# Performance work log

Hardware: AMD Instinct MI355X
Metric: run time of the kernel (lower is better)

The kernel has to match this reference:

```python
import jax, jax.numpy as jnp
import numpy as np

INPUT_SIZE = 512
HIDDEN = 1024
N_QP = 64
M_QP = 128
QP_ITER = 50
MIN_EIG = 0.01
N_P = N_QP * (N_QP + 1) // 2              # 2080
N_H = M_QP * N_QP                          # 8192
N_OUT = N_P + N_QP + N_H + M_QP            # 10464
BATCH = 1024


def setup_inputs() -> dict:
    key = jax.random.key(0)
    ks = jax.random.split(key, 4)
    s = lambda fan_in: np.float32(1.0 / np.sqrt(fan_in))
    return {
        "x": jax.random.normal(ks[0], (BATCH, INPUT_SIZE), jnp.float32),
        "W1": jax.random.normal(ks[1], (INPUT_SIZE, HIDDEN), jnp.float32) * s(INPUT_SIZE),
        "b1": jnp.zeros((HIDDEN,), jnp.float32),
        "W2": jax.random.normal(ks[2], (HIDDEN, HIDDEN), jnp.float32) * s(HIDDEN),
        "b2": jnp.zeros((HIDDEN,), jnp.float32),
        "W3": jax.random.normal(ks[3], (HIDDEN, N_OUT), jnp.float32) * s(HIDDEN),
        "b3": jnp.zeros((N_OUT,), jnp.float32),
    }


def _make_psd(p):
    # p: (bs, n(n+1)/2) packed row-major lower triangle of Cholesky factor L.
    # Diagonal entries (index i(i+1)/2 - 1) -> sqrt(min_eig) + softplus, so P = L L' is PSD.
    bs = p.shape[0]
    i = jnp.arange(1, N_QP + 1)
    diag_idx = i * (i + 1) // 2 - 1
    p = p.at[:, diag_idx].set(np.float32(np.sqrt(MIN_EIG)) + jax.nn.softplus(p[:, diag_idx]))
    r, c = jnp.tril_indices(N_QP)
    L = jnp.zeros((bs, N_QP, N_QP), p.dtype).at[:, r, c].set(p)
    return jnp.einsum('bik,bjk->bij', L, L)


def _forward(x, W1, b1, W2, b2, W3, b3):
    # MLP generating QP parameters (P, q, H, b)
    h = jax.nn.relu(x @ W1 + b1)
    h = jax.nn.relu(h @ W2 + b2)
    out = h @ W3 + b3                               # (bs, N_OUT)
    P_params = out[:, :N_P]
    q = out[:, N_P:N_P + N_QP]                      # (bs, n)
    H = out[:, N_P + N_QP:N_P + N_QP + N_H].reshape(-1, M_QP, N_QP)  # (bs, m, n)
    b = out[:, N_P + N_QP + N_H:]                   # (bs, m)
    P = _make_psd(P_params)                         # (bs, n, n)

    # Step sizes: tau = sigma = 0.9 / ||H||_2, spectral norm via 10 fixed power iterations
    v = jnp.ones((x.shape[0], N_QP), x.dtype) / np.float32(np.sqrt(N_QP))
    for _ in range(10):
        w = jnp.einsum('bmn,bm->bn', H, jnp.einsum('bmn,bn->bm', H, v))
        v = w / (jnp.linalg.norm(w, axis=1, keepdims=True) + 1e-12)
    sn = jnp.linalg.norm(jnp.einsum('bmn,bn->bm', H, v), axis=1) + 1e-6
    tau = (0.9 / sn)[:, None]                       # (bs, 1) primal step
    sig = tau                                       # dual step

    # Precompute (I + tau P)^{-1} once; fixed across PDHG iterations
    eye = jnp.eye(N_QP, dtype=x.dtype)
    Minv = jnp.linalg.inv(eye[None] + tau[:, :, None] * P)

    x0 = jnp.zeros((x.shape[0], N_QP), x.dtype)
    lam0 = jnp.zeros((x.shape[0], M_QP), x.dtype)

    def step(carry, _):
        xp, xbar, lam = carry
        lam = jax.nn.relu(lam - sig * (jnp.einsum('bmn,bn->bm', H, xbar) + b))
        xn = jnp.einsum('bnk,bk->bn', Minv, xp + tau * (jnp.einsum('bmn,bm->bn', H, lam) - q))
        return (xn, 2.0 * xn - xp, lam), None

    (xs, _, _), _ = jax.lax.scan(step, (x0, x0, lam0), None, length=QP_ITER)
    return xs  # (bs, n_qp): last primal iterate, matching solver(...)[1][:, -1, :]


def reference(x, W1, b1, W2, b2, W3, b3):
    return _forward(x, W1, b1, W2, b2, W3, b3)
```

## Files before the change

### kernel.cpp

```cpp
#include <hip/hip_runtime.h>
#include <cstdint>

typedef unsigned short u16;
typedef __attribute__((ext_vector_type(8))) short short8;
typedef __attribute__((ext_vector_type(4))) float floatx4;
typedef __attribute__((ext_vector_type(4))) float f4;

#define NQP   64
#define MQP   128
#define NP    2080
#define NHH   8192
#define NOUT  10464
#define NOUTP 10496

__device__ __forceinline__ float b2f(u16 u) {
  union { unsigned int i; float f; } v; v.i = ((unsigned int)u) << 16; return v.f;
}
__device__ __forceinline__ u16 f2b(float f) {
  union { float f; unsigned int i; } v; v.f = f;
  unsigned int r = v.i + 0x7fffu + ((v.i >> 16) & 1u);
  return (u16)(r >> 16);
}

__global__ __launch_bounds__(256) void detect_dtype(const u16* __restrict__ w,
                                                    int* __restrict__ flag) {
  __shared__ int cnt;
  if (threadIdx.x == 0) cnt = 0;
  __syncthreads();
  int c = 0;
  for (int i = threadIdx.x; i < 16384; i += 256) {
    const int e = (w[i] >> 7) & 0xFF;
    if (e >= 130 || e <= 90) ++c;
  }
  atomicAdd(&cnt, c);
  __syncthreads();
  if (threadIdx.x == 0) flag[0] = (cnt > 3000) ? 1 : 0;
}

__device__ __forceinline__ u16 load_elem_bf16(const void* p, size_t idx, int isf32) {
  return isf32 ? f2b(((const float*)p)[idx]) : ((const u16*)p)[idx];
}

__global__ __launch_bounds__(256) void convert_bf16(const void* __restrict__ in,
                                                    u16* __restrict__ out, int n,
                                                    const int* __restrict__ flag) {
  const int isf = flag[0];
  for (int i = blockIdx.x * 256 + threadIdx.x; i < n; i += gridDim.x * 256)
    out[i] = load_elem_bf16(in, i, isf);
}

__global__ __launch_bounds__(256) void conv_biases(const void* __restrict__ b1,
                                                   const void* __restrict__ b2,
                                                   const void* __restrict__ b3,
                                                   float* __restrict__ bf1,
                                                   float* __restrict__ bf2,
                                                   float* __restrict__ bf3,
                                                   const int* __restrict__ flag) {
  const int isf = flag[0];
  const int i = blockIdx.x * 256 + threadIdx.x;
  if (i < 1024) {
    bf1[i] = isf ? ((const float*)b1)[i] : b2f(((const u16*)b1)[i]);
  } else if (i < 2048) {
    const int j = i - 1024;
    bf2[j] = isf ? ((const float*)b2)[j] : b2f(((const u16*)b2)[j]);
  } else if (i < 2048 + NOUT) {
    const int j = i - 2048;
    bf3[j] = isf ? ((const float*)b3)[j] : b2f(((const u16*)b3)[j]);
  }
}

__global__ __launch_bounds__(256) void transpose_all(const void* __restrict__ W1,
                                                     const void* __restrict__ W2,
                                                     const void* __restrict__ W3,
                                                     u16* __restrict__ W1t,
                                                     u16* __restrict__ W2t,
                                                     u16* __restrict__ W3t,
                                                     const int* __restrict__ flag) {
  const int bx = blockIdx.x, by = blockIdx.y;
  const void* in; u16* out; int K, N, Npad, bxo;
  if (bx < 32)      { in = W1; out = W1t; K = 512;  N = 1024; Npad = 1024;  bxo = 0;
                      if (by >= 16) return; }
  else if (bx < 64) { in = W2; out = W2t; K = 1024; N = 1024; Npad = 1024;  bxo = 32; }
  else              { in = W3; out = W3t; K = 1024; N = NOUT; Npad = NOUTP; bxo = 64; }
  __shared__ u16 tile[32][33];
  const int isf = flag[0];
  const int n0 = (bx - bxo) * 32, k0 = by * 32;
  const int tx = threadIdx.x & 31, ty = threadIdx.x >> 5;
#pragma unroll
  for (int i = 0; i < 4; ++i) {
    const int k = k0 + ty + 8 * i, n = n0 + tx;
    tile[ty + 8 * i][tx] = (n < N) ? load_elem_bf16(in, (size_t)k * N + n, isf) : (u16)0;
  }
  __syncthreads();
#pragma unroll
  for (int i = 0; i < 4; ++i) {
    const int n = n0 + ty + 8 * i, k = k0 + tx;
    if (n < Npad) out[(size_t)n * K + k] = tile[tx][ty + 8 * i];
  }
}

__device__ __forceinline__ void gload_lds16(const u16* g, u16* l) {
  __builtin_amdgcn_global_load_lds((const __attribute__((address_space(1))) void*)g,
                                   (__attribute__((address_space(3))) void*)l, 16, 0, 0);
}

template <int EPI, bool HAS_LO>
__global__ __launch_bounds__(256) void gemm_bt(const u16* __restrict__ Ahi, const u16* __restrict__ Alo,
                                               const u16* __restrict__ Bt,  const float* __restrict__ bias,
                                               u16* __restrict__ Chi, u16* __restrict__ Clo,
                                               float* __restrict__ Cf,
                                               int M, int N, int K) {
  __shared__ __align__(16) u16 lA[128 * 32];
  __shared__ __align__(16) u16 lAlo[128 * 32];
  __shared__ __align__(16) u16 lB[128 * 32];
  const int tile_n = blockIdx.x * 128;
  const int tile_m = blockIdx.y * 128;
  const int lane = threadIdx.x & 63;
  const int wv   = threadIdx.x >> 6;
  const int wm = (wv & 1) * 64;
  const int wn = (wv >> 1) * 64;
  const int sr = lane >> 2;
  const int sk = (lane & 3) * 8;
  floatx4 acc[4][4] = {};

  for (int k0 = 0; k0 < K; k0 += 32) {
#pragma unroll
    for (int it = 0; it < 2; ++it) {
      const int slot = it * 4 + wv;
      const int r = slot * 16 + sr;
      gload_lds16(Ahi + (size_t)(tile_m + r) * K + k0 + sk, lA + slot * 512);
      if (HAS_LO)
        gload_lds16(Alo + (size_t)(tile_m + r) * K + k0 + sk, lAlo + slot * 512);
      gload_lds16(Bt + (size_t)(tile_n + r) * K + k0 + sk, lB + slot * 512);
    }
    __syncthreads();
    const int ro = lane & 15;
    const int qo = (lane >> 4) * 8;
    short8 af[4], bfr[4], al[4];
#pragma unroll
    for (int i = 0; i < 4; ++i) af[i] = *(const short8*)(lA + (wm + i * 16 + ro) * 32 + qo);
#pragma unroll
    for (int j = 0; j < 4; ++j) bfr[j] = *(const short8*)(lB + (wn + j * 16 + ro) * 32 + qo);
    if (HAS_LO) {
#pragma unroll
      for (int i = 0; i < 4; ++i) al[i] = *(const short8*)(lAlo + (wm + i * 16 + ro) * 32 + qo);
    }
#pragma unroll
    for (int i = 0; i < 4; ++i)
#pragma unroll
      for (int j = 0; j < 4; ++j) {
        acc[i][j] = __builtin_amdgcn_mfma_f32_16x16x32_bf16(af[i], bfr[j], acc[i][j], 0, 0, 0);
        if (HAS_LO)
          acc[i][j] = __builtin_amdgcn_mfma_f32_16x16x32_bf16(al[i], bfr[j], acc[i][j], 0, 0, 0);
      }
    __syncthreads();
  }

  const int colb = tile_n + wn + (lane & 15);
  const int rowb = tile_m + wm + (lane >> 4) * 4;
#pragma unroll
  for (int j = 0; j < 4; ++j) {
    const int col = colb + j * 16;
    const float bv = (col < N) ? bias[col] : 0.f;
#pragma unroll
    for (int i = 0; i < 4; ++i) {
#pragma unroll
      for (int v = 0; v < 4; ++v) {
        const int row = rowb + i * 16 + v;
        float val = acc[i][j][v] + bv;
        if (EPI == 0) {
          val = fmaxf(val, 0.f);
          const u16 hi = f2b(val);
          const float lo = val - b2f(hi);
          Chi[(size_t)row * N + col] = hi;
          Clo[(size_t)row * N + col] = f2b(lo);
        } else {
          if (col < N) Cf[(size_t)row * N + col] = val;
        }
      }
    }
  }
}

__device__ __forceinline__ f4 ld4s(const float* p) { return *(const f4*)p; }
__device__ __forceinline__ void st4s(float* p, f4 v) { *(f4*)p = v; }
__device__ __forceinline__ float dot4(f4 a, f4 b) {
  return fmaf(a.x, b.x, fmaf(a.y, b.y, fmaf(a.z, b.z, a.w * b.w)));
}
__device__ __forceinline__ f4 shx4(f4 v, int m) {
  f4 r;
  r.x = __shfl_xor(v.x, m, 64); r.y = __shfl_xor(v.y, m, 64);
  r.z = __shfl_xor(v.z, m, 64); r.w = __shfl_xor(v.w, m, 64);
  return r;
}
__device__ __forceinline__ int hQ(int m, int g) {
  return (m << 6) + (((g ^ (m & 15))) << 2);
}

__global__ __launch_bounds__(256, 4) void qp_solve(const float* __restrict__ outbuf,
                                                   void* __restrict__ xs,
                                                   const int* __restrict__ flag) {
  __shared__ __align__(16) float H_s[8192];
  __shared__ __align__(16) float lam_s[128];
  __shared__ __align__(16) float b_s[128];
  __shared__ __align__(16) float part_s[4][64];
  __shared__ __align__(16) float rhs_s[64];
  __shared__ __align__(16) float xb_s[64];
  __shared__ __align__(16) float xp_s[64];
  __shared__ __align__(16) float q_s[64];
  __shared__ __align__(16) float buf2[2][64];
  __shared__ float tau_sh;

  const int t = threadIdx.x;
  const int w = t >> 6, l = t & 63;
  const int am = 32 * w + (l >> 1), as = l & 1;
  const int bg = l & 15, bc = l >> 4;
  const int ci = 16 * w + (l >> 2), cc = l & 3;
  const int isf = flag[0];
  const float* ob = outbuf + (size_t)blockIdx.x * NOUT;

  float* Ld = H_s;
  float* ps = H_s + 4352;
  for (int e = t; e < 4352; e += 256) Ld[e] = 0.f;
  for (int e = t; e < NP; e += 256) ps[e] = ob[e];
  if (t < 64) q_s[t] = ob[NP + t];
  if (t >= 128 && t < 256) b_s[t - 128] = ob[NP + NQP + NHH + (t - 128)];
  __syncthreads();
  if (t < 64) {
    const int i = t + 1;
    const int d = i * (i + 1) / 2 - 1;
    const float xv = ps[d];
    ps[d] = 0.1f + (fmaxf(xv, 0.f) + log1pf(expf(-fabsf(xv))));
  }
  __syncthreads();
  for (int e = t; e < NP; e += 256) {
    int i = (int)((sqrtf(8.f * (float)e + 1.f) - 1.f) * 0.5f);
    while ((i + 1) * (i + 2) / 2 <= e) ++i;
    while (i * (i + 1) / 2 > e) --i;
    const int j = e - i * (i + 1) / 2;
    Ld[i * 68 + j] = ps[e];
  }
  __syncthreads();

  float M[16];
#pragma unroll
  for (int jj = 0; jj < 16; ++jj) M[jj] = 0.f;
#pragma unroll
  for (int h = 0; h < 2; ++h) {
    f4 Lr[8];
#pragma unroll
    for (int g = 0; g < 8; ++g) Lr[g] = ld4s(&Ld[ci * 68 + (h * 8 + g) * 4]);
#pragma unroll
    for (int jj = 0; jj < 16; ++jj) {
      const int j = 16 * cc + jj;
      float s = 0.f;
#pragma unroll
      for (int g = 0; g < 8; ++g) s += dot4(Lr[g], ld4s(&Ld[j * 68 + (h * 8 + g) * 4]));
      M[jj] += s;
    }
  }
  __syncthreads();

  for (int e = t; e < NHH; e += 256) {
    const int m = e >> 6, n = e & 63;
    H_s[hQ(m, n >> 2) + (n & 3)] = ob[NP + NQP + e];
  }
  if (t < 64) xb_s[t] = 0.125f;
  __syncthreads();

  for (int pi = 0; pi < 10; ++pi) {
    {
      float s = 0.f;
#pragma unroll
      for (int k = 0; k < 8; ++k) {
        const int g = 8 * as + k;
        s += dot4(ld4s(&H_s[hQ(am, g)]), ld4s(&xb_s[4 * g]));
      }
      s += __shfl_xor(s, 1, 64);
      if (as == 0) lam_s[am] = s;
    }
    __syncthreads();
    {
      f4 u = {0.f, 0.f, 0.f, 0.f};
#pragma unroll
      for (int k = 0; k < 8; ++k) {
        const int m = 32 * w + 8 * bc + k;
        u += ld4s(&H_s[hQ(m, bg)]) * lam_s[m];
      }
      u += shx4(u, 16); u += shx4(u, 32);
      if (l < 16) st4s(&part_s[w][4 * bg], u);
    }
    __syncthreads();
    if (t < 64) {
      const float u = part_s[0][t] + part_s[1][t] + part_s[2][t] + part_s[3][t];
      float ss = u * u;
#pragma unroll
      for (int o = 1; o <= 32; o <<= 1) ss += __shfl_xor(ss, o, 64);
      xb_s[t] = u / (sqrtf(ss) + 1e-12f);
    }
    __syncthreads();
  }
  {
    float s = 0.f;
#pragma unroll
    for (int k = 0; k < 8; ++k) {
      const int g = 8 * as + k;
      s += dot4(ld4s(&H_s[hQ(am, g)]), ld4s(&xb_s[4 * g]));
    }
    s += __shfl_xor(s, 1, 64);
    if (as == 0) lam_s[am] = s;
  }
  __syncthreads();
  if (t < 64) {
    const float a = lam_s[t], bb = lam_s[t + 64];
    float ss = a * a + bb * bb;
#pragma unroll
    for (int o = 1; o <= 32; o <<= 1) ss += __shfl_xor(ss, o, 64);
    if (t == 0) tau_sh = 0.9f / (sqrtf(ss) + 1e-6f);
  }
  __syncthreads();
  const float tau = tau_sh;

#pragma unroll
  for (int jj = 0; jj < 16; ++jj)
    M[jj] = tau * M[jj] + ((16 * cc + jj == ci) ? 1.0f : 0.0f);

  if (ci == 0) {
#pragma unroll
    for (int jj = 0; jj < 16; ++jj) buf2[0][16 * cc + jj] = M[jj];
  }
  __syncthreads();
#pragma unroll
  for (int k = 0; k < 64; ++k) {
    const int kb = k & 1;
    const int kc = k >> 4;
    const float d = 1.0f / buf2[kb][k];
    f4 rv[4];
#pragma unroll
    for (int u = 0; u < 4; ++u) rv[u] = ld4s(&buf2[kb][16 * cc + 4 * u]);
    const float f = __shfl(M[k & 15], (l & 60) | kc, 64);
    if (ci == k) {
#pragma unroll
      for (int jj = 0; jj < 16; ++jj) M[jj] = rv[jj >> 2][jj & 3] * d;
      if (cc == kc) M[k & 15] = d;
    } else {
#pragma unroll
      for (int jj = 0; jj < 16; ++jj)
        M[jj] = fmaf(-f, rv[jj >> 2][jj & 3] * d, M[jj]);
      if (cc == kc) M[k & 15] = -f * d;
    }
    if (k < 63 && ci == k + 1) {
#pragma unroll
      for (int jj = 0; jj < 16; ++jj) buf2[1 - kb][16 * cc + jj] = M[jj];
    }
    __syncthreads();
  }

  float c0;
  {
    float acc = 0.f;
#pragma unroll
    for (int u = 0; u < 4; ++u) {
      const f4 qv = ld4s(&q_s[16 * cc + 4 * u]);
      acc = fmaf(M[4 * u + 0], qv.x, acc);
      acc = fmaf(M[4 * u + 1], qv.y, acc);
      acc = fmaf(M[4 * u + 2], qv.z, acc);
      acc = fmaf(M[4 * u + 3], qv.w, acc);
    }
    acc += __shfl_xor(acc, 1, 64);
    acc += __shfl_xor(acc, 2, 64);
    c0 = tau * acc;
  }

  if (t < 64) { xb_s[t] = 0.f; xp_s[t] = 0.f; }
  float lam = 0.f, xpr = 0.f;
  const float br = b_s[am];
  __syncthreads();

  for (int it = 0; it < 50; ++it) {
    {
      float s = 0.f;
#pragma unroll
      for (int k = 0; k < 8; ++k) {
        const int g = 8 * as + k;
        s += dot4(ld4s(&H_s[hQ(am, g)]), ld4s(&xb_s[4 * g]));
      }
      s += __shfl_xor(s, 1, 64);
      lam = fmaxf(lam - tau * (s + br), 0.f);
      if (as == 0) lam_s[am] = lam;
    }
    __syncthreads();
    {
      f4 u = {0.f, 0.f, 0.f, 0.f};
#pragma unroll
      for (int k = 0; k < 8; ++k) {
        const int m = 32 * w + 8 * bc + k;
        u += ld4s(&H_s[hQ(m, bg)]) * lam_s[m];
      }
      u += shx4(u, 16); u += shx4(u, 32);
      if (l < 16) st4s(&part_s[w][4 * bg], u);
    }
    __syncthreads();
    if (t < 64) {
      const float uu = part_s[0][t] + part_s[1][t] + part_s[2][t] + part_s[3][t];
      rhs_s[t] = xp_s[t] + tau * uu;
    }
    __syncthreads();
    {
      float acc = 0.f;
#pragma unroll
      for (int u = 0; u < 4; ++u) {
        const f4 rv = ld4s(&rhs_s[16 * cc + 4 * u]);
        acc = fmaf(M[4 * u + 0], rv.x, acc);
        acc = fmaf(M[4 * u + 1], rv.y, acc);
        acc = fmaf(M[4 * u + 2], rv.z, acc);
        acc = fmaf(M[4 * u + 3], rv.w, acc);
      }
      acc += __shfl_xor(acc, 1, 64);
      acc += __shfl_xor(acc, 2, 64);
      if (cc == 0) {
        const float xn = acc - c0;
        xp_s[ci] = xn;
        xb_s[ci] = 2.f * xn - xpr;
        xpr = xn;
      }
    }
    __syncthreads();
  }

  if (cc == 0) {
    const size_t oi = (size_t)blockIdx.x * NQP + ci;
    if (isf) ((float*)xs)[oi] = xpr;
    else     ((u16*)xs)[oi]   = f2b(xpr);
  }
}

extern "C" void kernel_launch(void* const* d_in, const int* in_sizes, int n_in,
                              void* d_out, int out_size, void* d_ws, size_t ws_size,
                              hipStream_t stream) {
  const void* x  = d_in[0];
  const void* W1 = d_in[1];
  const void* b1 = d_in[2];
  const void* W2 = d_in[3];
  const void* b2 = d_in[4];
  const void* W3 = d_in[5];
  const void* b3 = d_in[6];

  char* ws = (char*)d_ws;
  size_t off = 0;
  auto take = [&](size_t bytes) -> char* {
    char* r = ws + off;
    off += (bytes + 255) & ~(size_t)255;
    return r;
  };
  int*   flag = (int*)take(256);
  float* bf1  = (float*)take(1024 * 4);
  float* bf2  = (float*)take(1024 * 4);
  float* bf3  = (float*)take((size_t)NOUT * 4);
  u16*   W3t  = (u16*)take((size_t)NOUTP * 1024 * 2);
  u16*   h2hi = (u16*)take(1024ull * 1024 * 2);
  u16*   h2lo = (u16*)take(1024ull * 1024 * 2);
  char*  region = take(1024ull * NOUT * 4);
  float* outf = (float*)region;
  u16* xb   = (u16*)(region + 0);
  u16* W1t  = (u16*)(region + (1u << 20));
  u16* W2t  = (u16*)(region + (2u << 20));
  u16* h1hi = (u16*)(region + (4u << 20));
  u16* h1lo = (u16*)(region + (6u << 20));
  (void)ws_size; (void)in_sizes; (void)n_in; (void)out_size;

  detect_dtype<<<dim3(1), 256, 0, stream>>>((const u16*)W1, flag);

  convert_bf16<<<dim3(512), 256, 0, stream>>>(x, xb, 1024 * 512, flag);
  conv_biases<<<dim3(49), 256, 0, stream>>>(b1, b2, b3, bf1, bf2, bf3, flag);
  transpose_all<<<dim3(392, 32), 256, 0, stream>>>(W1, W2, W3, W1t, W2t, W3t, flag);

  gemm_bt<0, false><<<dim3(8, 8), 256, 0, stream>>>(xb, nullptr, W1t, bf1,
                                                    h1hi, h1lo, nullptr, 1024, 1024, 512);
  gemm_bt<0, true><<<dim3(8, 8), 256, 0, stream>>>(h1hi, h1lo, W2t, bf2,
                                                   h2hi, h2lo, nullptr, 1024, 1024, 1024);
  gemm_bt<1, true><<<dim3(NOUTP / 128, 8), 256, 0, stream>>>(h2hi, h2lo, W3t, bf3,
                                                             nullptr, nullptr, outf, 1024, NOUT, 1024);
  qp_solve<<<dim3(1024), 256, 0, stream>>>(outf, d_out, flag);
}
```

Baseline: 505.5 us.

## Rewrite QP solver as single-wave blocks holding H and inverse in registers

The per-sample QP solver moves from 256-thread blocks with H staged in shared memory to 64-thread single-wavefront blocks. Each lane keeps two rows of H, a column of H transposed, and its row of P's inverse in registers. Gauss-Jordan inversion becomes row-per-lane, and the Cholesky product skips the zero upper triangle. This removes most shared-memory traffic and the cross-wave reductions in the iteration loop, at the cost of very high register pressure (about 200+ floats per lane, so spills are possible) and low thread-level parallelism per block.

After: 868.6 us. 1.72x slower.

```diff
diff --git a/kernel.cpp b/kernel.cpp
--- a/kernel.cpp
+++ b/kernel.cpp
@@ -12,6 +12,7 @@
 #define NHH   8192
 #define NOUT  10464
 #define NOUTP 10496
+#define HOFF  2144
 
 __device__ __forceinline__ float b2f(u16 u) {
   union { unsigned int i; float f; } v; v.i = ((unsigned int)u) << 16; return v.f;
@@ -187,252 +188,184 @@
 __device__ __forceinline__ float dot4(f4 a, f4 b) {
   return fmaf(a.x, b.x, fmaf(a.y, b.y, fmaf(a.z, b.z, a.w * b.w)));
 }
-__device__ __forceinline__ f4 shx4(f4 v, int m) {
-  f4 r;
-  r.x = __shfl_xor(v.x, m, 64); r.y = __shfl_xor(v.y, m, 64);
-  r.z = __shfl_xor(v.z, m, 64); r.w = __shfl_xor(v.w, m, 64);
-  return r;
-}
-__device__ __forceinline__ int hQ(int m, int g) {
-  return (m << 6) + (((g ^ (m & 15))) << 2);
-}
-
-__global__ __launch_bounds__(256, 4) void qp_solve(const float* __restrict__ outbuf,
-                                                   void* __restrict__ xs,
-                                                   const int* __restrict__ flag) {
-  __shared__ __align__(16) float H_s[8192];
-  __shared__ __align__(16) float lam_s[128];
-  __shared__ __align__(16) float b_s[128];
-  __shared__ __align__(16) float part_s[4][64];
-  __shared__ __align__(16) float rhs_s[64];
-  __shared__ __align__(16) float xb_s[64];
-  __shared__ __align__(16) float xp_s[64];
-  __shared__ __align__(16) float q_s[64];
-  __shared__ __align__(16) float buf2[2][64];
-  __shared__ float tau_sh;
-
-  const int t = threadIdx.x;
-  const int w = t >> 6, l = t & 63;
-  const int am = 32 * w + (l >> 1), as = l & 1;
-  const int bg = l & 15, bc = l >> 4;
-  const int ci = 16 * w + (l >> 2), cc = l & 3;
+
+__global__ __launch_bounds__(64, 1) void qp_solve(const float* __restrict__ outbuf,
+                                                  void* __restrict__ xs,
+                                                  const int* __restrict__ flag) {
+  __shared__ __align__(16) float Ld[64 * 68];
+  __shared__ __align__(16) float vec_s[64];
+  __shared__ __align__(16) float lam_sh[128];
+  __shared__ __align__(16) float rhs_sh[64];
+  __shared__ __align__(16) float q_sh[64];
+
+  const int l = threadIdx.x;
   const int isf = flag[0];
   const float* ob = outbuf + (size_t)blockIdx.x * NOUT;
 
-  float* Ld = H_s;
-  float* ps = H_s + 4352;
-  for (int e = t; e < 4352; e += 256) Ld[e] = 0.f;
-  for (int e = t; e < NP; e += 256) ps[e] = ob[e];
-  if (t < 64) q_s[t] = ob[NP + t];
-  if (t >= 128 && t < 256) b_s[t - 128] = ob[NP + NQP + NHH + (t - 128)];
-  __syncthreads();
-  if (t < 64) {
-    const int i = t + 1;
-    const int d = i * (i + 1) / 2 - 1;
-    const float xv = ps[d];
-    ps[d] = 0.1f + (fmaxf(xv, 0.f) + log1pf(expf(-fabsf(xv))));
-  }
-  __syncthreads();
-  for (int e = t; e < NP; e += 256) {
+  for (int e = l; e < 64 * 68; e += 64) Ld[e] = 0.f;
+  q_sh[l] = ob[NP + l];
+  __syncthreads();
+  for (int e = l; e < NP; e += 64) {
     int i = (int)((sqrtf(8.f * (float)e + 1.f) - 1.f) * 0.5f);
     while ((i + 1) * (i + 2) / 2 <= e) ++i;
     while (i * (i + 1) / 2 > e) --i;
     const int j = e - i * (i + 1) / 2;
-    Ld[i * 68 + j] = ps[e];
-  }
-  __syncthreads();
-
-  float M[16];
-#pragma unroll
-  for (int jj = 0; jj < 16; ++jj) M[jj] = 0.f;
-#pragma unroll
-  for (int h = 0; h < 2; ++h) {
-    f4 Lr[8];
-#pragma unroll
-    for (int g = 0; g < 8; ++g) Lr[g] = ld4s(&Ld[ci * 68 + (h * 8 + g) * 4]);
-#pragma unroll
-    for (int jj = 0; jj < 16; ++jj) {
-      const int j = 16 * cc + jj;
+    Ld[i * 68 + j] = ob[e];
+  }
+  __syncthreads();
+  {
+    const float xv = Ld[l * 68 + l];
+    Ld[l * 68 + l] = 0.1f + (fmaxf(xv, 0.f) + log1pf(expf(-fabsf(xv))));
+  }
+  __syncthreads();
+
+  f4 Mrow[16];
+  {
+    f4 Lr[17];
+#pragma unroll
+    for (int g = 0; g < 17; ++g) Lr[g] = ld4s(&Ld[l * 68 + 4 * g]);
+#pragma unroll
+    for (int j = 0; j < 64; ++j) {
       float s = 0.f;
 #pragma unroll
-      for (int g = 0; g < 8; ++g) s += dot4(Lr[g], ld4s(&Ld[j * 68 + (h * 8 + g) * 4]));
-      M[jj] += s;
-    }
-  }
-  __syncthreads();
-
-  for (int e = t; e < NHH; e += 256) {
-    const int m = e >> 6, n = e & 63;
-    H_s[hQ(m, n >> 2) + (n & 3)] = ob[NP + NQP + e];
-  }
-  if (t < 64) xb_s[t] = 0.125f;
-  __syncthreads();
-
+      for (int g = 0; g <= (j >> 2); ++g) s += dot4(Lr[g], ld4s(&Ld[j * 68 + 4 * g]));
+      Mrow[j >> 2][j & 3] = s;
+    }
+  }
+  __syncthreads();
+
+  f4 R0[16], R1[16], HT[32];
+#pragma unroll
+  for (int g = 0; g < 16; ++g) R0[g] = *(const f4*)(ob + HOFF + l * 64 + 4 * g);
+#pragma unroll
+  for (int g = 0; g < 16; ++g) R1[g] = *(const f4*)(ob + HOFF + (l + 64) * 64 + 4 * g);
+#pragma unroll
+  for (int mg = 0; mg < 32; ++mg) {
+    f4 h;
+    h.x = ob[HOFF + (4 * mg + 0) * 64 + l];
+    h.y = ob[HOFF + (4 * mg + 1) * 64 + l];
+    h.z = ob[HOFF + (4 * mg + 2) * 64 + l];
+    h.w = ob[HOFF + (4 * mg + 3) * 64 + l];
+    HT[mg] = h;
+  }
+  const float b0 = ob[HOFF + NHH + l];
+  const float b1 = ob[HOFF + NHH + 64 + l];
+
+  vec_s[l] = 0.125f;
+  __syncthreads();
   for (int pi = 0; pi < 10; ++pi) {
-    {
-      float s = 0.f;
-#pragma unroll
-      for (int k = 0; k < 8; ++k) {
-        const int g = 8 * as + k;
-        s += dot4(ld4s(&H_s[hQ(am, g)]), ld4s(&xb_s[4 * g]));
-      }
-      s += __shfl_xor(s, 1, 64);
-      if (as == 0) lam_s[am] = s;
-    }
-    __syncthreads();
-    {
-      f4 u = {0.f, 0.f, 0.f, 0.f};
-#pragma unroll
-      for (int k = 0; k < 8; ++k) {
-        const int m = 32 * w + 8 * bc + k;
-        u += ld4s(&H_s[hQ(m, bg)]) * lam_s[m];
-      }
-      u += shx4(u, 16); u += shx4(u, 32);
-      if (l < 16) st4s(&part_s[w][4 * bg], u);
-    }
-    __syncthreads();
-    if (t < 64) {
-      const float u = part_s[0][t] + part_s[1][t] + part_s[2][t] + part_s[3][t];
-      float ss = u * u;
-#pragma unroll
-      for (int o = 1; o <= 32; o <<= 1) ss += __shfl_xor(ss, o, 64);
-      xb_s[t] = u / (sqrtf(ss) + 1e-12f);
-    }
-    __syncthreads();
-  }
+    float s0 = 0.f, s1 = 0.f;
+#pragma unroll
+    for (int g = 0; g < 16; ++g) {
+      const f4 xv = ld4s(&vec_s[4 * g]);
+      s0 += dot4(R0[g], xv); s1 += dot4(R1[g], xv);
+    }
+    lam_sh[l] = s0; lam_sh[l + 64] = s1;
+    __syncthreads();
+    float u = 0.f;
+#pragma unroll
+    for (int mg = 0; mg < 32; ++mg) u += dot4(HT[mg], ld4s(&lam_sh[4 * mg]));
+    float ss = u * u;
+#pragma unroll
+    for (int o = 1; o <= 32; o <<= 1) ss += __shfl_xor(ss, o, 64);
+    vec_s[l] = u / (sqrtf(ss) + 1e-12f);
+    __syncthreads();
+  }
+  float tau;
   {
-    float s = 0.f;
-#pragma unroll
-    for (int k = 0; k < 8; ++k) {
-      const int g = 8 * as + k;
-      s += dot4(ld4s(&H_s[hQ(am, g)]), ld4s(&xb_s[4 * g]));
-    }
-    s += __shfl_xor(s, 1, 64);
-    if (as == 0) lam_s[am] = s;
-  }
-  __syncthreads();
-  if (t < 64) {
-    const float a = lam_s[t], bb = lam_s[t + 64];
-    float ss = a * a + bb * bb;
+    float s0 = 0.f, s1 = 0.f;
+#pragma unroll
+    for (int g = 0; g < 16; ++g) {
+      const f4 xv = ld4s(&vec_s[4 * g]);
+      s0 += dot4(R0[g], xv); s1 += dot4(R1[g], xv);
+    }
+    float ss = s0 * s0 + s1 * s1;
 #pragma unroll
     for (int o = 1; o <= 32; o <<= 1) ss += __shfl_xor(ss, o, 64);
-    if (t == 0) tau_sh = 0.9f / (sqrtf(ss) + 1e-6f);
-  }
-  __syncthreads();
-  const float tau = tau_sh;
-
-#pragma unroll
-  for (int jj = 0; jj < 16; ++jj)
-    M[jj] = tau * M[jj] + ((16 * cc + jj == ci) ? 1.0f : 0.0f);
-
-  if (ci == 0) {
-#pragma unroll
-    for (int jj = 0; jj < 16; ++jj) buf2[0][16 * cc + jj] = M[jj];
-  }
-  __syncthreads();
+    tau = 0.9f / (sqrtf(ss) + 1e-6f);
+  }
+
+#pragma unroll
+  for (int jg = 0; jg < 16; ++jg) {
+    f4 m = Mrow[jg] * tau;
+    m.x += (4 * jg + 0 == l) ? 1.f : 0.f;
+    m.y += (4 * jg + 1 == l) ? 1.f : 0.f;
+    m.z += (4 * jg + 2 == l) ? 1.f : 0.f;
+    m.w += (4 * jg + 3 == l) ? 1.f : 0.f;
+    Mrow[jg] = m;
+  }
+
 #pragma unroll
   for (int k = 0; k < 64; ++k) {
-    const int kb = k & 1;
-    const int kc = k >> 4;
-    const float d = 1.0f / buf2[kb][k];
-    f4 rv[4];
-#pragma unroll
-    for (int u = 0; u < 4; ++u) rv[u] = ld4s(&buf2[kb][16 * cc + 4 * u]);
-    const float f = __shfl(M[k & 15], (l & 60) | kc, 64);
-    if (ci == k) {
-#pragma unroll
-      for (int jj = 0; jj < 16; ++jj) M[jj] = rv[jj >> 2][jj & 3] * d;
-      if (cc == kc) M[k & 15] = d;
-    } else {
-#pragma unroll
-      for (int jj = 0; jj < 16; ++jj)
-        M[jj] = fmaf(-f, rv[jj >> 2][jj & 3] * d, M[jj]);
-      if (cc == kc) M[k & 15] = -f * d;
-    }
-    if (k < 63 && ci == k + 1) {
-#pragma unroll
-      for (int jj = 0; jj < 16; ++jj) buf2[1 - kb][16 * cc + jj] = M[jj];
-    }
+    if (l == k) {
+#pragma unroll
+      for (int jg = 0; jg < 16; ++jg) st4s(&rhs_sh[4 * jg], Mrow[jg]);
+    }
+    __syncthreads();
+    const float d = 1.0f / rhs_sh[k];
+    float f;
+    { const f4 mk = Mrow[k >> 2];
+      f = (k & 3) == 0 ? mk.x : (k & 3) == 1 ? mk.y : (k & 3) == 2 ? mk.z : mk.w; }
+    const bool piv = (l == k);
+#pragma unroll
+    for (int jg = 0; jg < 16; ++jg) {
+      const f4 srk = ld4s(&rhs_sh[4 * jg]) * d;
+      const f4 m = Mrow[jg];
+      f4 r;
+      r.x = piv ? srk.x : fmaf(-f, srk.x, m.x);
+      r.y = piv ? srk.y : fmaf(-f, srk.y, m.y);
+      r.z = piv ? srk.z : fmaf(-f, srk.z, m.z);
+      r.w = piv ? srk.w : fmaf(-f, srk.w, m.w);
+      Mrow[jg] = r;
+    }
+    { const float v = piv ? d : -f * d;
+      f4 mk = Mrow[k >> 2];
+      if ((k & 3) == 0) mk.x = v; else if ((k & 3) == 1) mk.y = v;
+      else if ((k & 3) == 2) mk.z = v; else mk.w = v;
+      Mrow[k >> 2] = mk; }
     __syncthreads();
   }
 
   float c0;
   {
-    float acc = 0.f;
-#pragma unroll
-    for (int u = 0; u < 4; ++u) {
-      const f4 qv = ld4s(&q_s[16 * cc + 4 * u]);
-      acc = fmaf(M[4 * u + 0], qv.x, acc);
-      acc = fmaf(M[4 * u + 1], qv.y, acc);
-      acc = fmaf(M[4 * u + 2], qv.z, acc);
-      acc = fmaf(M[4 * u + 3], qv.w, acc);
-    }
-    acc += __shfl_xor(acc, 1, 64);
-    acc += __shfl_xor(acc, 2, 64);
-    c0 = tau * acc;
-  }
-
-  if (t < 64) { xb_s[t] = 0.f; xp_s[t] = 0.f; }
-  float lam = 0.f, xpr = 0.f;
-  const float br = b_s[am];
-  __syncthreads();
-
+    float a = 0.f;
+#pragma unroll
+    for (int kg = 0; kg < 16; ++kg) a += dot4(Mrow[kg], ld4s(&q_sh[4 * kg]));
+    c0 = tau * a;
+  }
+
+  float lam0 = 0.f, lam1 = 0.f, xp = 0.f;
+  vec_s[l] = 0.f;
+  __syncthreads();
   for (int it = 0; it < 50; ++it) {
-    {
-      float s = 0.f;
-#pragma unroll
-      for (int k = 0; k < 8; ++k) {
-        const int g = 8 * as + k;
-        s += dot4(ld4s(&H_s[hQ(am, g)]), ld4s(&xb_s[4 * g]));
-      }
-      s += __shfl_xor(s, 1, 64);
-      lam = fmaxf(lam - tau * (s + br), 0.f);
-      if (as == 0) lam_s[am] = lam;
-    }
-    __syncthreads();
-    {
-      f4 u = {0.f, 0.f, 0.f, 0.f};
-#pragma unroll
-      for (int k = 0; k < 8; ++k) {
-        const int m = 32 * w + 8 * bc + k;
-        u += ld4s(&H_s[hQ(m, bg)]) * lam_s[m];
-      }
-      u += shx4(u, 16); u += shx4(u, 32);
-      if (l < 16) st4s(&part_s[w][4 * bg], u);
-    }
-    __syncthreads();
-    if (t < 64) {
-      const float uu = part_s[0][t] + part_s[1][t] + part_s[2][t] + part_s[3][t];
-      rhs_s[t] = xp_s[t] + tau * uu;
-    }
-    __syncthreads();
-    {
-      float acc = 0.f;
-#pragma unroll
-      for (int u = 0; u < 4; ++u) {
-        const f4 rv = ld4s(&rhs_s[16 * cc + 4 * u]);
-        acc = fmaf(M[4 * u + 0], rv.x, acc);
-        acc = fmaf(M[4 * u + 1], rv.y, acc);
-        acc = fmaf(M[4 * u + 2], rv.z, acc);
-        acc = fmaf(M[4 * u + 3], rv.w, acc);
-      }
-      acc += __shfl_xor(acc, 1, 64);
-      acc += __shfl_xor(acc, 2, 64);
-      if (cc == 0) {
-        const float xn = acc - c0;
-        xp_s[ci] = xn;
-        xb_s[ci] = 2.f * xn - xpr;
-        xpr = xn;
-      }
-    }
-    __syncthreads();
-  }
-
-  if (cc == 0) {
-    const size_t oi = (size_t)blockIdx.x * NQP + ci;
-    if (isf) ((float*)xs)[oi] = xpr;
-    else     ((u16*)xs)[oi]   = f2b(xpr);
-  }
+    float s0 = 0.f, s1 = 0.f;
+#pragma unroll
+    for (int g = 0; g < 16; ++g) {
+      const f4 xv = ld4s(&vec_s[4 * g]);
+      s0 += dot4(R0[g], xv); s1 += dot4(R1[g], xv);
+    }
+    lam0 = fmaxf(lam0 - tau * (s0 + b0), 0.f);
+    lam1 = fmaxf(lam1 - tau * (s1 + b1), 0.f);
+    lam_sh[l] = lam0; lam_sh[l + 64] = lam1;
+    __syncthreads();
+    float u = 0.f;
+#pragma unroll
+    for (int mg = 0; mg < 32; ++mg) u += dot4(HT[mg], ld4s(&lam_sh[4 * mg]));
+    rhs_sh[l] = xp + tau * u;
+    __syncthreads();
+    float xn = 0.f;
+#pragma unroll
+    for (int kg = 0; kg < 16; ++kg) xn += dot4(Mrow[kg], ld4s(&rhs_sh[4 * kg]));
+    xn -= c0;
+    __syncthreads();
+    vec_s[l] = 2.f * xn - xp;
+    xp = xn;
+    __syncthreads();
+  }
+
+  const size_t oi = (size_t)blockIdx.x * NQP + l;
+  if (isf) ((float*)xs)[oi] = xp;
+  else     ((u16*)xs)[oi]   = f2b(xp);
 }
 
 extern "C" void kernel_launch(void* const* d_in, const int* in_sizes, int n_in,
@@ -481,5 +414,5 @@
                                                    h2hi, h2lo, nullptr, 1024, 1024, 1024);
   gemm_bt<1, true><<<dim3(NOUTP / 128, 8), 256, 0, stream>>>(h2hi, h2lo, W3t, bf3,
                                                              nullptr, nullptr, outf, 1024, NOUT, 1024);
-  qp_solve<<<dim3(1024), 256, 0, stream>>>(outf, d_out, flag);
-}
+  qp_solve<<<dim3(1024), 64, 0, stream>>>(outf, d_out, flag);
+}
```
